# Optimization experiments

Measured on AMD Instinct MI355X. Metric: run time of the kernel, lower is better.

Reference implementation:

```python
import jax, jax.numpy as jnp
import numpy as np

B, D = 8192, 512
MARGIN, CR_BETA, NUM_CLASSES = 0.2, 0.1, 1000


def setup_inputs() -> dict:
    key = jax.random.key(0)
    k1, k2, k3, k4 = jax.random.split(key, 4)
    return {
        "img": jax.random.normal(k1, (B, D), jnp.float32),
        "txt": jax.random.normal(k2, (B, D), jnp.float32),
        "txt_cr": jax.random.normal(k3, (B, D), jnp.float32),
        "labels": jax.random.randint(k4, (B,), 0, NUM_CLASSES),
        "auto_margin_flag": 1,
        "margin": jnp.full((B,), MARGIN, jnp.float32),  # opt.margin repeated per row
        "cr_beta": CR_BETA,
    }


def _similarity(a, b):
    # row-normalize then full cosine-similarity matrix + matched (diagonal) sims
    an = a / (jnp.linalg.norm(a, axis=1, keepdims=True) + 1e-8)
    bn = b / (jnp.linalg.norm(b, axis=1, keepdims=True) + 1e-8)
    return an @ bn.T, jnp.sum(an * bn, axis=1)


def _dir_loss(sim, labels, margin, auto_flag):
    # semi-hard negative mining per anchor row, fully vectorized.
    # Deterministic stand-in for np.random.choice: first valid negative index.
    diag = jnp.diagonal(sim)                               # sim[idx, idx]
    neg_mask = labels[None, :] != labels[:, None]          # [B,B] negatives
    loss_mat = sim - diag[:, None] + margin[:, None]       # triplet margin term
    valid = neg_mask & (loss_mat > 0) & (loss_mat < margin[:, None])
    valid = jax.lax.stop_gradient(valid)                   # mining is detached (numpy in torch)
    has_valid = jnp.any(valid, axis=1)
    if auto_flag:
        row_ok = (margin >= 0.16) & has_valid
    else:
        row_ok = has_valid
    neg_idx = jnp.argmax(valid, axis=1)                    # first valid negative
    sim_an = jnp.take_along_axis(sim, neg_idx[:, None], axis=1)[:, 0]
    per_row = jax.nn.relu(margin - diag + sim_an)
    return jnp.sum(jnp.where(row_ok, per_row, 0.0))


def _cr_loss(img, txt, txt_cr, labels, auto_flag, margin, cr_beta):
    sim, sm = _similarity(img, txt)
    sim_cr, sm_cr = _similarity(img, txt_cr)
    if auto_flag:
        lam = jnp.abs(jax.lax.stop_gradient(sm_cr)) / jnp.abs(jax.lax.stop_gradient(sm))
        lam = jnp.minimum(lam, 1.0)                        # clamp lambda_cr to <= 1
        margin_cr = (lam + 1.0) * margin / 2.0
    else:
        margin_cr = margin / 2.0
    margin_cr = jax.lax.stop_gradient(margin_cr)
    base = _dir_loss(sim, labels, margin, auto_flag) + _dir_loss(sim.T, labels, margin, auto_flag)
    cr = _dir_loss(sim_cr, labels, margin_cr, auto_flag) + _dir_loss(sim_cr.T, labels, margin_cr, auto_flag)
    return base + cr_beta * cr


def reference(img, txt, txt_cr, labels, auto_margin_flag, margin, cr_beta):
    return _cr_loss(img, txt, txt_cr, labels, bool(auto_margin_flag), margin, cr_beta)
```

## Files before the change

kernel.cpp:

```cpp
#include <hip/hip_runtime.h>
#include <climits>

#define NB 8192
#define ND 512

#define WCHUNKS 32
#define WTILES 4
#define WCAP (WTILES * 64)
#define WCOLS (64 + WCHUNKS * 32)
#define TCHUNKS ((NB - 64) / 32)
#define TFB 64
#define TFTOT (TFB * 4)

#define PK_NONE (~0ULL)

__device__ inline unsigned long long pack_cand(int col, float lm) {
    return ((unsigned long long)(unsigned)col << 32) |
           (unsigned long long)__float_as_uint(lm);
}


__global__ __launch_bounds__(256) void stats_k(
        const float* __restrict__ img, const float* __restrict__ txt,
        const float* __restrict__ cr, const float* __restrict__ margin,
        const int* __restrict__ flagp,
        float* rnImg, float* rnTxt, float* rnCr,
        float* dgSim, float* dgCr, float* mgCr,
        unsigned long long* negIdx64, int* stragCnt, float* out) {
    int tid = threadIdx.x, bid = blockIdx.x;
    int g = bid * 256 + tid;
    if (g < 4 * NB) negIdx64[g] = PK_NONE;
    if (bid == 0 && tid < 16) stragCnt[tid] = 0;
    if (bid == 0 && tid == 0) out[0] = 0.0f;

    int r = bid * 16 + (tid >> 4);
    int q = tid & 15;
    const float4* iv = (const float4*)(img + (size_t)r * ND);
    const float4* tv = (const float4*)(txt + (size_t)r * ND);
    const float4* cv = (const float4*)(cr  + (size_t)r * ND);
    float sii = 0, stt = 0, scc = 0, sit = 0, sic = 0;
    #pragma unroll
    for (int i = 0; i < 8; ++i) {
        int k = q + i * 16;
        float4 x = iv[k], y = tv[k], w = cv[k];
        sii += x.x*x.x + x.y*x.y + x.z*x.z + x.w*x.w;
        stt += y.x*y.x + y.y*y.y + y.z*y.z + y.w*y.w;
        scc += w.x*w.x + w.y*w.y + w.z*w.z + w.w*w.w;
        sit += x.x*y.x + x.y*y.y + x.z*y.z + x.w*y.w;
        sic += x.x*w.x + x.y*w.y + x.z*w.z + x.w*w.w;
    }
    #pragma unroll
    for (int off = 1; off < 16; off <<= 1) {
        sii += __shfl_xor(sii, off); stt += __shfl_xor(stt, off);
        scc += __shfl_xor(scc, off); sit += __shfl_xor(sit, off);
        sic += __shfl_xor(sic, off);
    }
    if (q == 0) {
        float rnI = 1.0f / (sqrtf(sii) + 1e-8f);
        float rnT = 1.0f / (sqrtf(stt) + 1e-8f);
        float rnC = 1.0f / (sqrtf(scc) + 1e-8f);
        float ds = sit * rnI * rnT;
        float dc = sic * rnI * rnC;
        float m  = margin[r];
        float mcr = flagp[0] ? (fminf(fabsf(dc) / fabsf(ds), 1.0f) + 1.0f) * m * 0.5f
                             : m * 0.5f;
        rnImg[r] = rnI; rnTxt[r] = rnT; rnCr[r] = rnC;
        dgSim[r] = ds;  dgCr[r]  = dc;  mgCr[r] = mcr;
    }
}

__device__ inline void pass_arrays(int z,
        const float* img, const float* txt, const float* cr,
        const float* rnImg, const float* rnTxt, const float* rnCr,
        const float* dgSim, const float* dgCr,
        const float* margin, const float* mgCr,
        const float*& A, const float*& B, const float*& rnA, const float*& rnB,
        const float*& dgA, const float*& mgA) {
    if (z == 0)      { A = img; B = txt; rnA = rnImg; rnB = rnTxt; dgA = dgSim; mgA = margin; }
    else if (z == 1) { A = txt; B = img; rnA = rnTxt; rnB = rnImg; dgA = dgSim; mgA = margin; }
    else if (z == 2) { A = img; B = cr;  rnA = rnImg; rnB = rnCr;  dgA = dgCr;  mgA = mgCr;   }
    else             { A = cr;  B = img; rnA = rnCr;  rnB = rnImg; dgA = dgCr;  mgA = mgCr;   }
}

__global__ __launch_bounds__(256) void band_k(
        const float* __restrict__ img, const float* __restrict__ txt,
        const float* __restrict__ cr, const int* __restrict__ labels,
        const int* __restrict__ flagp, const float* __restrict__ margin,
        const float* __restrict__ betap,
        const float* rnImg, const float* rnTxt, const float* rnCr,
        const float* dgSim, const float* dgCr, const float* mgCr,
        int* stragCnt, int* stragList, float* out) {
    __shared__ __align__(16) float As[16][68];
    __shared__ __align__(16) float Bs[16][68];
    __shared__ float aRn[64], aDg[64], aMg[64], colRn[64];
    __shared__ int   aLab[64], colLab[64], resIdx[64];
    __shared__ float blockAcc;

    const int tid = threadIdx.x, z = blockIdx.y, a0 = blockIdx.x * 64;
    const int flag = flagp[0];
    const float *A, *B, *rnA, *rnB, *dgA, *mgA;
    pass_arrays(z, img, txt, cr, rnImg, rnTxt, rnCr, dgSim, dgCr, margin, mgCr,
                A, B, rnA, rnB, dgA, mgA);

    if (tid < 64) {
        int a = a0 + tid;
        float mg = mgA[a];
        aRn[tid] = rnA[a]; aDg[tid] = dgA[a]; aMg[tid] = mg;
        aLab[tid] = labels[a];
        colRn[tid] = rnB[tid]; colLab[tid] = labels[tid];
        resIdx[tid] = (flag && mg < 0.16f) ? -1 : INT_MAX;
    }
    if (tid == 0) blockAcc = 0.0f;

    const int ty4  = (tid >> 4) * 4, tx4 = (tid & 15) * 4;
    const int lrow = tid >> 2,  lk4 = (tid & 3) * 4;

    float acc[4][4];
    #pragma unroll
    for (int i = 0; i < 4; ++i)
        #pragma unroll
        for (int j = 0; j < 4; ++j) acc[i][j] = 0.0f;

    float4 va = *(const float4*)(A + (size_t)(a0 + lrow) * ND + lk4);
    float4 vb = *(const float4*)(B + (size_t)lrow * ND + lk4);
    for (int kc = 0; kc < ND; kc += 16) {
        __syncthreads();
        As[lk4 + 0][lrow] = va.x; As[lk4 + 1][lrow] = va.y;
        As[lk4 + 2][lrow] = va.z; As[lk4 + 3][lrow] = va.w;
        Bs[lk4 + 0][lrow] = vb.x; Bs[lk4 + 1][lrow] = vb.y;
        Bs[lk4 + 2][lrow] = vb.z; Bs[lk4 + 3][lrow] = vb.w;
        if (kc + 16 < ND) {
            va = *(const float4*)(A + (size_t)(a0 + lrow) * ND + kc + 16 + lk4);
            vb = *(const float4*)(B + (size_t)lrow * ND + kc + 16 + lk4);
        }
        __syncthreads();
        #pragma unroll
        for (int k = 0; k < 16; ++k) {
            float4 av = *(const float4*)&As[k][ty4];
            float4 bv = *(const float4*)&Bs[k][tx4];
            float ar[4] = {av.x, av.y, av.z, av.w};
            float br[4] = {bv.x, bv.y, bv.z, bv.w};
            #pragma unroll
            for (int i = 0; i < 4; ++i)
                #pragma unroll
                for (int j = 0; j < 4; ++j)
                    acc[i][j] = fmaf(ar[i], br[j], acc[i][j]);
        }
    }
    __syncthreads();

    #pragma unroll
    for (int i = 0; i < 4; ++i) {
        int r = ty4 + i;
        float mgv = aMg[r];
        if (flag && mgv < 0.16f) continue;
        float dg = aDg[r], rna = aRn[r];
        int la = aLab[r];
        #pragma unroll
        for (int j = 0; j < 4; ++j) {
            int c = tx4 + j;
            if (colLab[c] == la) continue;
            float lm = acc[i][j] * rna * colRn[c] - dg + mgv;
            if (lm > 0.0f && lm < mgv) atomicMin(&resIdx[r], c);
        }
    }
    __syncthreads();

    #pragma unroll
    for (int i = 0; i < 4; ++i) {
        int r = ty4 + i;
        int w = resIdx[r];
        if (w < 0 || w == INT_MAX) continue;
        int c = w - tx4;
        if (c < 0 || c > 3) continue;
        float lm = acc[i][c] * aRn[r] * colRn[w] - aDg[r] + aMg[r];
        atomicAdd(&blockAcc, lm);
    }
    __syncthreads();

    if (tid < 64 && resIdx[tid] == INT_MAX) {
        int pos = atomicAdd(&stragCnt[z], 1);
        stragList[z * NB + pos] = a0 + tid;
    }
    if (tid == 0 && blockAcc != 0.0f) {
        float scale = (z >= 2) ? betap[0] : 1.0f;
        atomicAdd(out, blockAcc * scale);
    }
}

__global__ __launch_bounds__(256) void wina_k(
        const float* __restrict__ img, const float* __restrict__ txt,
        const float* __restrict__ cr, const int* __restrict__ labels,
        const float* __restrict__ margin,
        const float* rnImg, const float* rnTxt, const float* rnCr,
        const float* dgSim, const float* dgCr, const float* mgCr,
        const int* stragCnt, const int* stragList,
        unsigned long long* negIdx64) {
    __shared__ __align__(16) float As[16][68];
    __shared__ __align__(16) float Bs[16][36];
    __shared__ float aRn[64], aDg[64], aMg[64], colRn[32];
    __shared__ int   aId[64], aRow[64], aLab[64], colLab[32];

    const int tid = threadIdx.x, z = blockIdx.y;
    const int chunk = blockIdx.x & (WCHUNKS - 1);
    const int t     = blockIdx.x / WCHUNKS;
    int cnt = stragCnt[z];
    if (cnt <= 0) return;
    cnt = min(cnt, NB);
    if (t * 64 >= cnt) return;
    const int c0 = 64 + chunk * 32;

    const float *A, *B, *rnA, *rnB, *dgA, *mgA;
    pass_arrays(z, img, txt, cr, rnImg, rnTxt, rnCr, dgSim, dgCr, margin, mgCr,
                A, B, rnA, rnB, dgA, mgA);

    if (tid < 64) {
        int s = t * 64 + tid;
        int a = (s < cnt) ? stragList[z * NB + s] : -1;
        if ((unsigned)a >= NB) a = -1;
        int ar = (a >= 0) ? a : 0;
        aId[tid] = a; aRow[tid] = ar;
        aRn[tid] = rnA[ar]; aDg[tid] = dgA[ar]; aMg[tid] = mgA[ar];
        aLab[tid] = labels[ar];
    }
    if (tid < 32) { colRn[tid] = rnB[c0 + tid]; colLab[tid] = labels[c0 + tid]; }
    __syncthreads();

    const int ty4  = (tid >> 4) * 4, tx2 = (tid & 15) * 2;
    const int lrow = tid >> 2,  lk4 = (tid & 3) * 4;
    const int arow = aRow[lrow];
    const bool doB = tid < 128;

    float acc[4][2];
    #pragma unroll
    for (int i = 0; i < 4; ++i) { acc[i][0] = 0.0f; acc[i][1] = 0.0f; }

    float4 va = *(const float4*)(A + (size_t)arow * ND + lk4);
    float4 vb;
    if (doB) vb = *(const float4*)(B + (size_t)(c0 + lrow) * ND + lk4);
    for (int kc = 0; kc < ND; kc += 16) {
        __syncthreads();
        As[lk4 + 0][lrow] = va.x; As[lk4 + 1][lrow] = va.y;
        As[lk4 + 2][lrow] = va.z; As[lk4 + 3][lrow] = va.w;
        if (doB) {
            Bs[lk4 + 0][lrow] = vb.x; Bs[lk4 + 1][lrow] = vb.y;
            Bs[lk4 + 2][lrow] = vb.z; Bs[lk4 + 3][lrow] = vb.w;
        }
        if (kc + 16 < ND) {
            va = *(const float4*)(A + (size_t)arow * ND + kc + 16 + lk4);
            if (doB) vb = *(const float4*)(B + (size_t)(c0 + lrow) * ND + kc + 16 + lk4);
        }
        __syncthreads();
        #pragma unroll
        for (int k = 0; k < 16; ++k) {
            float4 av = *(const float4*)&As[k][ty4];
            float2 bv = *(const float2*)&Bs[k][tx2];
            float ar[4] = {av.x, av.y, av.z, av.w};
            #pragma unroll
            for (int i = 0; i < 4; ++i) {
                acc[i][0] = fmaf(ar[i], bv.x, acc[i][0]);
                acc[i][1] = fmaf(ar[i], bv.y, acc[i][1]);
            }
        }
    }
    __syncthreads();

    #pragma unroll
    for (int i = 0; i < 4; ++i) {
        int r = ty4 + i;
        int a = aId[r];
        if (a < 0) continue;
        float dg = aDg[r], mgv = aMg[r], rna = aRn[r];
        int la = aLab[r];
        #pragma unroll
        for (int j = 0; j < 2; ++j) {
            int c = tx2 + j;
            if (colLab[c] == la) continue;
            float lm = acc[i][j] * rna * colRn[c] - dg + mgv;
            if (lm > 0.0f && lm < mgv)
                atomicMin(&negIdx64[z * NB + a], pack_cand(c0 + c, lm));
        }
    }
}

__device__ inline float dot8(const float4& a0, const float4& a1,
                             const float4& b0, const float4& b1) {
    return a0.x*b0.x + a0.y*b0.y + a0.z*b0.z + a0.w*b0.w
         + a1.x*b1.x + a1.y*b1.y + a1.z*b1.z + a1.w*b1.w;
}

__global__ __launch_bounds__(256) void tailfin_k(
        const float* __restrict__ img, const float* __restrict__ txt,
        const float* __restrict__ cr, const int* __restrict__ labels,
        const float* __restrict__ margin, const float* __restrict__ betap,
        const float* rnImg, const float* rnTxt, const float* rnCr,
        const float* dgSim, const float* dgCr, const float* mgCr,
        const int* stragCnt, const int* stragList,
        unsigned long long* negIdx64, int* arrive, float* out) {
    __shared__ __align__(16) float Aload[8][ND];
    __shared__ float sRn[8], sDg[8], sMg[8];
    __shared__ int   sLab[8], sAid[8];
    __shared__ float colRn_s[32];
    __shared__ int   colLab_s[32];
    __shared__ int   sSurv[256];
    __shared__ int   sNa;
    __shared__ int   sLast;
    __shared__ float fS4[4];

    const int tid = threadIdx.x, z = blockIdx.y, bx = blockIdx.x;
    int cnt = stragCnt[z];
    cnt = (cnt < 0) ? 0 : min(cnt, NB);

    const float *A, *B, *rnA, *rnB, *dgA, *mgA;
    pass_arrays(z, img, txt, cr, rnImg, rnTxt, rnCr, dgSim, dgCr,
                margin, mgCr, A, B, rnA, rnB, dgA, mgA);

    if (tid == 0) sNa = 0;
    __syncthreads();
    for (int s = tid; s < cnt; s += 256) {
        int a = stragList[z * NB + s];
        if ((unsigned)a < NB && negIdx64[z * NB + a] == PK_NONE) {
            int p = atomicAdd(&sNa, 1);
            if (p < 256) sSurv[p] = a;
        }
    }
    __syncthreads();
    const int na = min(sNa, 256);

    if (na > 0) {
        const int wv = tid >> 6, lane = tid & 63;
        for (int ci = 0; ci < (TCHUNKS + TFB - 1) / TFB; ++ci) {
            const int chunk = bx + ci * TFB;
            if (chunk >= TCHUNKS) break;
            const int c0 = 64 + chunk * 32;
            if (cnt <= WCAP && c0 < WCOLS) continue;
            __syncthreads();
            if (tid < 32) { colRn_s[tid] = rnB[c0 + tid]; colLab_s[tid] = labels[c0 + tid]; }

            for (int g0 = 0; g0 < na; g0 += 8) {
                const int gn = min(8, na - g0);
                __syncthreads();
                if (tid < 8) {
                    int s = g0 + ((tid < gn) ? tid : 0);
                    int a = sSurv[s];
                    sAid[tid] = (tid < gn) ? a : -1;
                    sRn[tid] = rnA[a]; sDg[tid] = dgA[a]; sMg[tid] = mgA[a];
                    sLab[tid] = labels[a];
                }
                #pragma unroll
                for (int m = 0; m < 4; ++m) {
                    int idx = tid + m * 256;
                    int row = idx >> 7, f4 = idx & 127;
                    if (row < gn) {
                        int a = sSurv[g0 + row];
                        *(float4*)&Aload[row][f4 * 4] =
                            *(const float4*)(A + (size_t)a * ND + f4 * 4);
                    }
                }
                __syncthreads();

                #pragma unroll
                for (int cb = 0; cb < 2; ++cb) {
                    const int cc0 = wv * 8 + cb * 4;
                    float4 b0[4], b1[4];
                    #pragma unroll
                    for (int q = 0; q < 4; ++q) {
                        const float4* Bv = (const float4*)(B + (size_t)(c0 + cc0 + q) * ND);
                        b0[q] = Bv[lane]; b1[q] = Bv[lane + 64];
                    }
                    for (int s = 0; s < gn; ++s) {
                        float4 a0v = *(const float4*)&Aload[s][lane * 4];
                        float4 a1v = *(const float4*)&Aload[s][(lane + 64) * 4];
                        float d0 = dot8(a0v, a1v, b0[0], b1[0]);
                        float d1 = dot8(a0v, a1v, b0[1], b1[1]);
                        float d2 = dot8(a0v, a1v, b0[2], b1[2]);
                        float d3 = dot8(a0v, a1v, b0[3], b1[3]);
                        #pragma unroll
                        for (int off = 1; off < 64; off <<= 1) {
                            d0 += __shfl_xor(d0, off); d1 += __shfl_xor(d1, off);
                            d2 += __shfl_xor(d2, off); d3 += __shfl_xor(d3, off);
                        }
                        if (lane == 0) {
                            int aid = sAid[s];
                            float rn = sRn[s], dg = sDg[s], mg = sMg[s];
                            int lb = sLab[s];
                            float dv[4] = {d0, d1, d2, d3};
                            #pragma unroll
                            for (int q = 0; q < 4; ++q) {
                                int cc = cc0 + q;
                                if (colLab_s[cc] != lb) {
                                    float lm = dv[q] * rn * colRn_s[cc] - dg + mg;
                                    if (lm > 0.0f && lm < mg)
                                        atomicMin(&negIdx64[z * NB + aid],
                                                  pack_cand(c0 + cc, lm));
                                }
                            }
                        }
                    }
                }
            }
        }
    }

    __syncthreads();
    if (tid == 0) {
        asm volatile("s_waitcnt vmcnt(0)" ::: "memory");
        int old = atomicAdd(arrive, 1);
        sLast = (old == TFTOT - 1) ? 1 : 0;
    }
    __syncthreads();
    if (!sLast) return;

    float total = 0.0f;
    for (int zz = 0; zz < 4; ++zz) {
        int c2 = stragCnt[zz];
        c2 = (c2 < 0) ? 0 : min(c2, NB);
        float scale = (zz >= 2) ? betap[0] : 1.0f;
        for (int t = tid; t < c2; t += 256) {
            int a = stragList[zz * NB + t];
            if ((unsigned)a >= NB) continue;
            unsigned long long pk = atomicMin(&negIdx64[zz * NB + a], PK_NONE);
            if (pk == PK_NONE) continue;
            unsigned col = (unsigned)(pk >> 32);
            if (col >= NB) continue;
            float lm = __uint_as_float((unsigned)(pk & 0xFFFFFFFFu));
            total += lm * scale;
        }
    }
    #pragma unroll
    for (int off = 32; off; off >>= 1) total += __shfl_xor(total, off);
    if ((tid & 63) == 0) fS4[tid >> 6] = total;
    __syncthreads();
    if (tid == 0) {
        float sum = fS4[0] + fS4[1] + fS4[2] + fS4[3];
        if (sum != 0.0f) atomicAdd(out, sum);
    }
}


__global__ __launch_bounds__(256) void zero_k(float* out, int n) {
    int g = blockIdx.x * 256 + threadIdx.x;
    if (g < n) out[g] = 0.0f;
}

template <int U>
__device__ void stragScan(const float* __restrict__ A, const float* __restrict__ B,
                          const int* __restrict__ labels, int a0, int u, int scol,
                          const int* sList, int g0,
                          const float* aRn, const float* aDg, const float* aMg,
                          const int* aLab, int* sMin8, int* doneMask,
                          float* blockAcc) {
    const int tid = threadIdx.x;
    float rn_s[U], dg_s[U], mg_s[U];
    int lab_s[U];
    const float4* Av[U];
    #pragma unroll
    for (int s = 0; s < U; ++s) {
        int slot = sList[g0 + (s < u ? s : 0)];
        rn_s[s] = aRn[slot]; dg_s[s] = aDg[slot]; mg_s[s] = aMg[slot];
        lab_s[s] = aLab[slot];
        Av[s] = (const float4*)(A + (size_t)(a0 + slot) * ND);
    }
    if (tid < U) sMin8[tid] = INT_MAX;
    if (tid == 0) *doneMask = 0;
    __syncthreads();
    for (int jb = scol; jb < NB; jb += 256) {
        int j = jb + tid;
        bool jv = (j < NB);
        int mask = *doneMask;
        float dot[U];
        #pragma unroll
        for (int s = 0; s < U; ++s) dot[s] = 0.0f;
        float ssq = 0.0f;
        if (jv) {
            const float4* Bv = (const float4*)(B + (size_t)j * ND);
            #pragma unroll 4
            for (int k4 = 0; k4 < ND / 4; ++k4) {
                float4 b = Bv[k4];
                ssq += b.x*b.x + b.y*b.y + b.z*b.z + b.w*b.w;
                #pragma unroll
                for (int s = 0; s < U; ++s) {
                    float4 a = Av[s][k4];
                    dot[s] += a.x*b.x + a.y*b.y + a.z*b.z + a.w*b.w;
                }
            }
        }
        float rnb = 1.0f / (sqrtf(ssq) + 1e-8f);
        int lj = jv ? labels[j] : -1;
        float lmv[U];
        #pragma unroll
        for (int s = 0; s < U; ++s) {
            lmv[s] = dot[s] * rn_s[s] * rnb - dg_s[s] + mg_s[s];
            if (jv && s < u && !((mask >> s) & 1) && lj != lab_s[s] &&
                lmv[s] > 0.0f && lmv[s] < mg_s[s])
                atomicMin(&sMin8[s], j);
        }
        __syncthreads();
        #pragma unroll
        for (int s = 0; s < U; ++s)
            if (jv && s < u && !((mask >> s) & 1) && sMin8[s] == j)
                atomicAdd(blockAcc, lmv[s]);
        __syncthreads();
        if (tid == 0) {
            int m2 = 0;
            for (int s = 0; s < u; ++s)
                if (sMin8[s] != INT_MAX) m2 |= (1 << s);
            *doneMask = m2;
        }
        __syncthreads();
        if (*doneMask == (1 << u) - 1) break;
    }
}

__global__ __launch_bounds__(256) void mine_k(const float* __restrict__ img,
                                              const float* __restrict__ txt,
                                              const float* __restrict__ cr,
                                              const int*   __restrict__ labels,
                                              const int*   __restrict__ flagp,
                                              const float* __restrict__ margin,
                                              const float* __restrict__ betap,
                                              float* __restrict__ out) {
    __shared__ __align__(16) float As[16][64];
    __shared__ __align__(16) float Bs[16][64];
    __shared__ float aRn[64], aDg[64], aMg[64];
    __shared__ int   aLab[64];
    __shared__ float colRn[64];
    __shared__ int   colLab[64];
    __shared__ int   resIdx[64], prevIdx[64];
    __shared__ int   cnt;
    __shared__ float blockAcc;
    __shared__ int   sList[64];
    __shared__ int   sCnt;
    __shared__ int   sMin8[8];
    __shared__ int   doneMask;

    const int tid  = threadIdx.x;
    const int z    = blockIdx.y;
    const int a0   = blockIdx.x * 64;
    const int flag = flagp[0];
    const float* A = (z == 1) ? txt : (z == 3) ? cr : img;
    const float* B = (z == 0) ? txt : (z == 2) ? cr : img;
    {
        int ar = tid >> 2, q = tid & 3;
        int a  = a0 + ar;
        const float4* iv = (const float4*)(img + (size_t)a * ND) + q * 32;
        const float4* tv = (const float4*)(txt + (size_t)a * ND) + q * 32;
        const float4* cv = (const float4*)(cr  + (size_t)a * ND) + q * 32;
        float sii = 0, stt = 0, scc = 0, sit = 0, sic = 0;
        #pragma unroll 4
        for (int i = 0; i < 32; ++i) {
            float4 x = iv[i], y = tv[i], w = cv[i];
            sii += x.x*x.x + x.y*x.y + x.z*x.z + x.w*x.w;
            stt += y.x*y.x + y.y*y.y + y.z*y.z + y.w*y.w;
            scc += w.x*w.x + w.y*w.y + w.z*w.z + w.w*w.w;
            sit += x.x*y.x + x.y*y.y + x.z*y.z + x.w*y.w;
            sic += x.x*w.x + x.y*w.y + x.z*w.z + x.w*w.w;
        }
        sii += __shfl_xor(sii, 1); sii += __shfl_xor(sii, 2);
        stt += __shfl_xor(stt, 1); stt += __shfl_xor(stt, 2);
        sit += __shfl_xor(sit, 1); sit += __shfl_xor(sit, 2);
        scc += __shfl_xor(scc, 1); scc += __shfl_xor(scc, 2);
        sic += __shfl_xor(sic, 1); sic += __shfl_xor(sic, 2);
        if (q == 0) {
            float rnI = 1.0f / (sqrtf(sii) + 1e-8f);
            float rnT = 1.0f / (sqrtf(stt) + 1e-8f);
            float ds  = sit * rnI * rnT;
            float m   = margin[a];
            float mg, rna, dgv;
            if (z >= 2) {
                float rnC = 1.0f / (sqrtf(scc) + 1e-8f);
                float dc  = sic * rnI * rnC;
                mg = flag ? (fminf(fabsf(dc) / fabsf(ds), 1.0f) + 1.0f) * m * 0.5f
                          : m * 0.5f;
                dgv = dc; rna = (z == 3) ? rnC : rnI;
            } else {
                mg = m; dgv = ds; rna = (z == 1) ? rnT : rnI;
            }
            aRn[ar] = rna; aDg[ar] = dgv; aMg[ar] = mg; aLab[ar] = labels[a];
            resIdx[ar] = (flag && mg < 0.16f) ? -1 : INT_MAX;
        }
        if (tid == 0) blockAcc = 0.0f;
    }
    __syncthreads();
    const int ty4  = (tid >> 4) * 4, tx4 = (tid & 15) * 4;
    const int lrow = tid >> 2,  lk4 = (tid & 3) * 4;
    int bandCols = 0, unresolved = 64;
    for (int jc = 0; jc < 2; ++jc) {
        int j0 = jc * 64;
        float acc[4][4];
        #pragma unroll
        for (int i = 0; i < 4; ++i)
            #pragma unroll
            for (int j = 0; j < 4; ++j) acc[i][j] = 0.0f;
        float bssq = 0.0f;
        for (int kc = 0; kc < ND; kc += 16) {
            __syncthreads();
            float4 va = *(const float4*)(A + (size_t)(a0 + lrow) * ND + kc + lk4);
            float4 vb = *(const float4*)(B + (size_t)(j0 + lrow) * ND + kc + lk4);
            As[lk4 + 0][lrow] = va.x; As[lk4 + 1][lrow] = va.y;
            As[lk4 + 2][lrow] = va.z; As[lk4 + 3][lrow] = va.w;
            Bs[lk4 + 0][lrow] = vb.x; Bs[lk4 + 1][lrow] = vb.y;
            Bs[lk4 + 2][lrow] = vb.z; Bs[lk4 + 3][lrow] = vb.w;
            bssq += vb.x*vb.x + vb.y*vb.y + vb.z*vb.z + vb.w*vb.w;
            __syncthreads();
            #pragma unroll
            for (int k = 0; k < 16; ++k) {
                float4 av = *(const float4*)&As[k][ty4];
                float4 bv = *(const float4*)&Bs[k][tx4];
                float ar[4] = {av.x, av.y, av.z, av.w};
                float br[4] = {bv.x, bv.y, bv.z, bv.w};
                #pragma unroll
                for (int i = 0; i < 4; ++i)
                    #pragma unroll
                    for (int j = 0; j < 4; ++j)
                        acc[i][j] = fmaf(ar[i], br[j], acc[i][j]);
            }
        }
        bssq += __shfl_xor(bssq, 1); bssq += __shfl_xor(bssq, 2);
        __syncthreads();
        if ((tid & 3) == 0) {
            colRn[lrow]  = 1.0f / (sqrtf(bssq) + 1e-8f);
            colLab[lrow] = labels[j0 + lrow];
        }
        if (tid < 64) prevIdx[tid] = resIdx[tid];
        __syncthreads();
        #pragma unroll
        for (int i = 0; i < 4; ++i) {
            int r = ty4 + i;
            if (prevIdx[r] != INT_MAX) continue;
            float dg = aDg[r], mgv = aMg[r], rna = aRn[r];
            int la = aLab[r];
            #pragma unroll
            for (int j = 0; j < 4; ++j) {
                int c = tx4 + j;
                if (colLab[c] == la) continue;
                float v  = acc[i][j] * rna * colRn[c];
                float lm = v - dg + mgv;
                if (lm > 0.0f && lm < mgv) atomicMin(&resIdx[r], j0 + c);
            }
        }
        __syncthreads();
        #pragma unroll
        for (int i = 0; i < 4; ++i) {
            int r = ty4 + i;
            if (prevIdx[r] != INT_MAX) continue;
            int w = resIdx[r];
            if (w == INT_MAX) continue;
            int c = w - j0 - tx4;
            if (c < 0 || c > 3) continue;
            float v  = acc[i][c] * aRn[r] * colRn[tx4 + c];
            float lm = v - aDg[r] + aMg[r];
            atomicAdd(&blockAcc, lm);
        }
        __syncthreads();
        if (tid == 0) cnt = 0;
        __syncthreads();
        if (tid < 64 && resIdx[tid] == INT_MAX) atomicAdd(&cnt, 1);
        __syncthreads();
        unresolved = cnt;
        bandCols = j0 + 64;
        __syncthreads();
        if (unresolved <= 8) break;
    }
    if (unresolved > 0) {
        if (tid == 0) sCnt = 0;
        __syncthreads();
        if (tid < 64 && resIdx[tid] == INT_MAX) {
            int pos = atomicAdd(&sCnt, 1);
            sList[pos] = tid;
        }
        __syncthreads();
        int total = sCnt;
        for (int g0 = 0; g0 < total; g0 += 8) {
            int u = min(8, total - g0);
            if (u == 1)      stragScan<1>(A, B, labels, a0, u, bandCols, sList, g0, aRn, aDg, aMg, aLab, sMin8, &doneMask, &blockAcc);
            else if (u == 2) stragScan<2>(A, B, labels, a0, u, bandCols, sList, g0, aRn, aDg, aMg, aLab, sMin8, &doneMask, &blockAcc);
            else if (u <= 4) stragScan<4>(A, B, labels, a0, u, bandCols, sList, g0, aRn, aDg, aMg, aLab, sMin8, &doneMask, &blockAcc);
            else             stragScan<8>(A, B, labels, a0, u, bandCols, sList, g0, aRn, aDg, aMg, aLab, sMin8, &doneMask, &blockAcc);
            __syncthreads();
        }
    }
    if (tid == 0 && blockAcc != 0.0f) {
        float scale = (z >= 2) ? betap[0] : 1.0f;
        atomicAdd(out, blockAcc * scale);
    }
}


extern "C" void kernel_launch(void* const* d_in, const int* in_sizes, int n_in,
                              void* d_out, int out_size, void* d_ws, size_t ws_size,
                              hipStream_t stream) {
    const float* img    = (const float*)d_in[0];
    const float* txt    = (const float*)d_in[1];
    const float* cr     = (const float*)d_in[2];
    const int*   labels = (const int*)  d_in[3];
    const int*   flagp  = (const int*)  d_in[4];
    const float* marg   = (const float*)d_in[5];
    const float* betap  = (const float*)d_in[6];
    float* out = (float*)d_out;
    (void)in_sizes; (void)n_in;

    const size_t REQ = (size_t)(6 * NB) * 4 + (size_t)(4 * NB) * 8 + 64 +
                       (size_t)(4 * NB) * 4;
    if (ws_size >= REQ) {
        float* wf = (float*)d_ws;
        float* rnImg = wf + 0 * NB;
        float* rnTxt = wf + 1 * NB;
        float* rnCr  = wf + 2 * NB;
        float* dgSim = wf + 3 * NB;
        float* dgCr  = wf + 4 * NB;
        float* mgCr  = wf + 5 * NB;
        unsigned long long* negIdx64 = (unsigned long long*)(wf + 6 * NB);
        int* stragCnt  = (int*)(negIdx64 + 4 * NB);
        int* stragList = stragCnt + 16;
        int* arrive    = stragCnt + 8;

        stats_k  <<<dim3(NB / 16),             dim3(256), 0, stream>>>(
            img, txt, cr, marg, flagp,
            rnImg, rnTxt, rnCr, dgSim, dgCr, mgCr, negIdx64, stragCnt, out);
        band_k   <<<dim3(NB / 64, 4),          dim3(256), 0, stream>>>(
            img, txt, cr, labels, flagp, marg, betap,
            rnImg, rnTxt, rnCr, dgSim, dgCr, mgCr, stragCnt, stragList, out);
        wina_k   <<<dim3(WCHUNKS * WTILES, 4), dim3(256), 0, stream>>>(
            img, txt, cr, labels, marg,
            rnImg, rnTxt, rnCr, dgSim, dgCr, mgCr,
            stragCnt, stragList, negIdx64);
        tailfin_k<<<dim3(TFB, 4),              dim3(256), 0, stream>>>(
            img, txt, cr, labels, marg, betap,
            rnImg, rnTxt, rnCr, dgSim, dgCr, mgCr,
            stragCnt, stragList, negIdx64, arrive, out);
    } else {
        zero_k<<<dim3((out_size + 255) / 256), dim3(256), 0, stream>>>(out, out_size);
        mine_k<<<dim3(NB / 64, 4), dim3(256), 0, stream>>>(img, txt, cr, labels,
                                                           flagp, marg, betap, out);
    }
}
```

Before: 240.6 us.

## Restructure tail straggler scan to one column per thread with register dot products

After: 269.0 us. +11.8%, slower.

```diff
diff --git a/kernel.cpp b/kernel.cpp
--- a/kernel.cpp
+++ b/kernel.cpp
@@ -8,9 +8,8 @@
 #define WTILES 4
 #define WCAP (WTILES * 64)
 #define WCOLS (64 + WCHUNKS * 32)
-#define TCHUNKS ((NB - 64) / 32)
-#define TFB 64
-#define TFTOT (TFB * 4)
+#define TC2 32
+#define TFTOT (TC2 * 4)
 
 #define PK_NONE (~0ULL)
 
@@ -283,12 +282,6 @@
     }
 }
 
-__device__ inline float dot8(const float4& a0, const float4& a1,
-                             const float4& b0, const float4& b1) {
-    return a0.x*b0.x + a0.y*b0.y + a0.z*b0.z + a0.w*b0.w
-         + a1.x*b1.x + a1.y*b1.y + a1.z*b1.z + a1.w*b1.w;
-}
-
 __global__ __launch_bounds__(256) void tailfin_k(
         const float* __restrict__ img, const float* __restrict__ txt,
         const float* __restrict__ cr, const int* __restrict__ labels,
@@ -297,11 +290,6 @@
         const float* dgSim, const float* dgCr, const float* mgCr,
         const int* stragCnt, const int* stragList,
         unsigned long long* negIdx64, int* arrive, float* out) {
-    __shared__ __align__(16) float Aload[8][ND];
-    __shared__ float sRn[8], sDg[8], sMg[8];
-    __shared__ int   sLab[8], sAid[8];
-    __shared__ float colRn_s[32];
-    __shared__ int   colLab_s[32];
     __shared__ int   sSurv[256];
     __shared__ int   sNa;
     __shared__ int   sLast;
@@ -327,76 +315,52 @@
     __syncthreads();
     const int na = min(sNa, 256);
 
-    if (na > 0) {
-        const int wv = tid >> 6, lane = tid & 63;
-        for (int ci = 0; ci < (TCHUNKS + TFB - 1) / TFB; ++ci) {
-            const int chunk = bx + ci * TFB;
-            if (chunk >= TCHUNKS) break;
-            const int c0 = 64 + chunk * 32;
-            if (cnt <= WCAP && c0 < WCOLS) continue;
-            __syncthreads();
-            if (tid < 32) { colRn_s[tid] = rnB[c0 + tid]; colLab_s[tid] = labels[c0 + tid]; }
-
-            for (int g0 = 0; g0 < na; g0 += 8) {
-                const int gn = min(8, na - g0);
-                __syncthreads();
-                if (tid < 8) {
-                    int s = g0 + ((tid < gn) ? tid : 0);
-                    int a = sSurv[s];
-                    sAid[tid] = (tid < gn) ? a : -1;
-                    sRn[tid] = rnA[a]; sDg[tid] = dgA[a]; sMg[tid] = mgA[a];
-                    sLab[tid] = labels[a];
+    const int c0 = 64 + bx * 256;
+    const bool chunkCovered = (cnt <= WCAP) && (c0 + 256 <= WCOLS);
+    if (na > 0 && !chunkCovered) {
+        int j = c0 + tid;
+        bool jv = (j < NB);
+        if (cnt <= WCAP && j < WCOLS) jv = false;
+        int lj = 0; float rnb = 0.0f;
+        const float4* Bv = (const float4*)B;
+        if (jv) {
+            lj = labels[j]; rnb = rnB[j];
+            Bv = (const float4*)(B + (size_t)j * ND);
+        }
+        for (int g0 = 0; g0 < na; g0 += 8) {
+            const int gn = min(8, na - g0);
+            const float4* Av[8];
+            float rn_s[8], dg_s[8], mg_s[8];
+            int lab_s[8], aid_s[8];
+            #pragma unroll
+            for (int s = 0; s < 8; ++s) {
+                int a = sSurv[g0 + ((s < gn) ? s : 0)];
+                aid_s[s] = a;
+                rn_s[s] = rnA[a]; dg_s[s] = dgA[a]; mg_s[s] = mgA[a];
+                lab_s[s] = labels[a];
+                Av[s] = (const float4*)(A + (size_t)a * ND);
+            }
+            if (jv) {
+                float dot[8];
+                #pragma unroll
+                for (int s = 0; s < 8; ++s) dot[s] = 0.0f;
+                #pragma unroll 4
+                for (int k4 = 0; k4 < ND / 4; ++k4) {
+                    float4 b = Bv[k4];
+                    #pragma unroll
+                    for (int s = 0; s < 8; ++s) {
+                        float4 a = Av[s][k4];
+                        dot[s] += a.x*b.x + a.y*b.y + a.z*b.z + a.w*b.w;
+                    }
                 }
                 #pragma unroll
-                for (int m = 0; m < 4; ++m) {
-                    int idx = tid + m * 256;
-                    int row = idx >> 7, f4 = idx & 127;
-                    if (row < gn) {
-                        int a = sSurv[g0 + row];
-                        *(float4*)&Aload[row][f4 * 4] =
-                            *(const float4*)(A + (size_t)a * ND + f4 * 4);
-                    }
-                }
-                __syncthreads();
-
-                #pragma unroll
-                for (int cb = 0; cb < 2; ++cb) {
-                    const int cc0 = wv * 8 + cb * 4;
-                    float4 b0[4], b1[4];
-                    #pragma unroll
-                    for (int q = 0; q < 4; ++q) {
-                        const float4* Bv = (const float4*)(B + (size_t)(c0 + cc0 + q) * ND);
-                        b0[q] = Bv[lane]; b1[q] = Bv[lane + 64];
-                    }
-                    for (int s = 0; s < gn; ++s) {
-                        float4 a0v = *(const float4*)&Aload[s][lane * 4];
-                        float4 a1v = *(const float4*)&Aload[s][(lane + 64) * 4];
-                        float d0 = dot8(a0v, a1v, b0[0], b1[0]);
-                        float d1 = dot8(a0v, a1v, b0[1], b1[1]);
-                        float d2 = dot8(a0v, a1v, b0[2], b1[2]);
-                        float d3 = dot8(a0v, a1v, b0[3], b1[3]);
-                        #pragma unroll
-                        for (int off = 1; off < 64; off <<= 1) {
-                            d0 += __shfl_xor(d0, off); d1 += __shfl_xor(d1, off);
-                            d2 += __shfl_xor(d2, off); d3 += __shfl_xor(d3, off);
-                        }
-                        if (lane == 0) {
-                            int aid = sAid[s];
-                            float rn = sRn[s], dg = sDg[s], mg = sMg[s];
-                            int lb = sLab[s];
-                            float dv[4] = {d0, d1, d2, d3};
-                            #pragma unroll
-                            for (int q = 0; q < 4; ++q) {
-                                int cc = cc0 + q;
-                                if (colLab_s[cc] != lb) {
-                                    float lm = dv[q] * rn * colRn_s[cc] - dg + mg;
-                                    if (lm > 0.0f && lm < mg)
-                                        atomicMin(&negIdx64[z * NB + aid],
-                                                  pack_cand(c0 + cc, lm));
-                                }
-                            }
-                        }
-                    }
+                for (int s = 0; s < 8; ++s) {
+                    if (s >= gn) break;
+                    if (lj == lab_s[s]) continue;
+                    float lm = dot[s] * rn_s[s] * rnb - dg_s[s] + mg_s[s];
+                    if (lm > 0.0f && lm < mg_s[s])
+                        atomicMin(&negIdx64[z * NB + aid_s[s]],
+                                  pack_cand(j, lm));
                 }
             }
         }
@@ -725,7 +689,7 @@
             img, txt, cr, labels, marg,
             rnImg, rnTxt, rnCr, dgSim, dgCr, mgCr,
             stragCnt, stragList, negIdx64);
-        tailfin_k<<<dim3(TFB, 4),              dim3(256), 0, stream>>>(
+        tailfin_k<<<dim3(TC2, 4),              dim3(256), 0, stream>>>(
             img, txt, cr, labels, marg, betap,
             rnImg, rnTxt, rnCr, dgSim, dgCr, mgCr,
             stragCnt, stragList, negIdx64, arrive, out);
```
